# Kernel optimization log

Measured on AMD Instinct MI355X. Metric: run time of the kernel, lower is better.

Reference implementation:

```python
import jax, jax.numpy as jnp
import numpy as np

N, G, S = 51200, 128, 400  # nodes, graphs, nodes-per-graph
E, IN, H, OUT = 819200, 128, 128, 10


def _graph_conv(x, src, dst, W_rel, b_rel, W_root):
    # PyG GraphConv (aggr='add'): lin_rel(sum_{j->i} x_j) + lin_root(x_i)
    agg = jax.ops.segment_sum(x[src], dst, num_segments=N)  # [N, d]
    return agg @ W_rel + b_rel + x @ W_root


def _mixup(x, lam, perm):
    return x * lam + (1.0 - lam) * x[perm]


def setup_inputs() -> dict:
    key = jax.random.key(0)
    ks = jax.random.split(key, 12)
    rng = np.random.default_rng(0)

    x0 = jax.random.normal(ks[0], (N, IN), dtype=jnp.float32)
    edge_index = jax.random.randint(ks[1], (2, E), 0, N, dtype=jnp.int64)
    lam = jax.random.uniform(ks[2], (1,), dtype=jnp.float32)
    ptr = jnp.arange(0, N + 1, S, dtype=jnp.int64)            # [G+1]
    batch = jnp.repeat(jnp.arange(G, dtype=jnp.int64), S)     # [N]

    def seg_perm():
        return jnp.asarray(np.concatenate(
            [g * S + rng.permutation(S) for g in range(G)]), dtype=jnp.int64)

    perm1, perm2, perm3 = seg_perm(), seg_perm(), seg_perm()

    def lin(k, fan_in, fan_out):
        bound = 1.0 / np.sqrt(fan_in)
        return jax.random.uniform(k, (fan_in, fan_out), jnp.float32, -bound, bound)

    params = {
        'W1_rel': lin(ks[3], IN, H), 'b1_rel': jnp.zeros((H,), jnp.float32),
        'W1_root': lin(ks[4], IN, H),
        'W2_rel': lin(ks[5], H, H), 'b2_rel': jnp.zeros((H,), jnp.float32),
        'W2_root': lin(ks[6], H, H),
        'W_lin': lin(ks[7], H, OUT), 'b_lin': jnp.zeros((OUT,), jnp.float32),
    }
    return dict(x0=x0, edge_index=edge_index, lam=lam, ptr=ptr, batch=batch,
                perm1=perm1, perm2=perm2, perm3=perm3, **params)


def reference(x0, edge_index, lam, ptr, batch, perm1, perm2, perm3,
              W1_rel, b1_rel, W1_root, W2_rel, b2_rel, W2_root, W_lin, b_lin):
    src, dst = edge_index[0], edge_index[1]
    l = lam[0]

    x1 = jax.nn.relu(_graph_conv(x0, src, dst, W1_rel, b1_rel, W1_root))
    x1 = _mixup(x1, l, perm1)  # dropout p=0.4 is identity in eval mode

    x2 = jax.nn.relu(_graph_conv(x1, src, dst, W2_rel, b2_rel, W2_root))
    x2 = _mixup(x2, l, perm2)

    # NOTE: original forward reuses conv2 for the third layer (conv3 unused)
    x3 = jax.nn.relu(_graph_conv(x2, src, dst, W2_rel, b2_rel, W2_root))
    x3 = _mixup(x3, l, perm3)

    pooled = jax.ops.segment_sum(x3, batch, num_segments=G)  # [G, H]
    logits = pooled @ W_lin + b_lin                          # [G, OUT]
    return jax.nn.log_softmax(logits, axis=-1)
```

## Files before the change

kernel.cpp:

```cpp
#include <hip/hip_runtime.h>

#define N_NODES 51200
#define N_EDGES 819200
#define HDIM 128
#define AK 256
#define NGRAPH 128
#define SEG 400
#define NOUT 10
#define SLOT 64

typedef unsigned short ushort_t;
typedef unsigned int uint_t;
typedef __attribute__((ext_vector_type(8))) short bf16x8;
typedef __attribute__((ext_vector_type(16))) float f32x16;

static __device__ __forceinline__ unsigned short f2bf(float f) {
    unsigned int u = __float_as_uint(f);
    unsigned int r = (u + 0x7fffu + ((u >> 16) & 1u)) >> 16;
    return (unsigned short)r;
}
static __device__ __forceinline__ float bf2f(unsigned short h) {
    return __uint_as_float(((unsigned int)h) << 16);
}


__global__ void k_scatter(const int* __restrict__ src, const int* __restrict__ dst,
                          int* __restrict__ cnt, ushort_t* __restrict__ col2) {
    int e = blockIdx.x * 256 + threadIdx.x;
    int d = dst[e];
    int pos = atomicAdd(&cnt[d], 1);
    col2[(size_t)d * SLOT + pos] = (ushort_t)src[e];
}


__global__ void k_prep(const float* __restrict__ x, ushort_t* __restrict__ Abuf,
                       const float* __restrict__ W1rel, const float* __restrict__ W1root,
                       const float* __restrict__ W2rel, const float* __restrict__ W2root,
                       ushort_t* __restrict__ Wfrag1, ushort_t* __restrict__ Wfrag2,
                       float* __restrict__ pooled) {
    int b = blockIdx.x;
    if (b < 6400) {
        int idx = b * 256 + threadIdx.x;
        int row = idx >> 5;
        int c4 = (idx & 31) * 4;
        float4 v = *(const float4*)(x + (size_t)row * HDIM + c4);
        ushort4 h;
        h.x = f2bf(v.x); h.y = f2bf(v.y); h.z = f2bf(v.z); h.w = f2bf(v.w);
        *(ushort4*)(Abuf + (size_t)row * AK + HDIM + c4) = h;
    } else if (b < 6656) {
        int w2 = (b >= 6528);
        int tid = (b - (w2 ? 6528 : 6400)) * 256 + threadIdx.x;
        const float* Wrel  = w2 ? W2rel : W1rel;
        const float* Wroot = w2 ? W2root : W1root;
        ushort_t* dstF     = w2 ? Wfrag2 : Wfrag1;
        int j = tid & 7;
        int l = (tid >> 3) & 63;
        int s = (tid >> 9) & 15;
        int t = tid >> 13;
        int k = 16 * s + (l >> 5) * 8 + j;
        int n = 32 * t + (l & 31);
        float v = (k < HDIM) ? Wrel[(size_t)k * HDIM + n]
                             : Wroot[(size_t)(k - HDIM) * HDIM + n];
        dstF[tid] = f2bf(v);
    } else {
        int i = (b - 6656) * 256 + threadIdx.x;
        pooled[i] = 0.f;
    }
}


__global__ __launch_bounds__(256) void k_aggregate(ushort_t* __restrict__ Abuf,
                                                   const int* __restrict__ cnt,
                                                   const ushort_t* __restrict__ col) {
    int wave = threadIdx.x >> 6;
    int lane = threadIdx.x & 63;
    int il = lane & 15;
    int qe = lane >> 4;
    int node = blockIdx.x * 4 + wave;
    int beg = node * SLOT;
    int end = beg + cnt[node];

    const ushort_t* xsrc = Abuf + HDIM + (size_t)il * 8;

    float a[4][8];
#pragma unroll
    for (int j = 0; j < 4; ++j)
#pragma unroll
        for (int k = 0; k < 8; ++k) a[j][k] = 0.f;

    int e = beg;
    for (; e + 16 <= end; e += 16) {
        int c[4];
#pragma unroll
        for (int j = 0; j < 4; ++j) c[j] = (int)col[e + 4 * j + qe];
#pragma unroll
        for (int j = 0; j < 4; ++j) {
            uint4 v = *(const uint4*)(xsrc + (size_t)c[j] * AK);
            a[j][0] += __uint_as_float(v.x << 16);
            a[j][1] += __uint_as_float(v.x & 0xffff0000u);
            a[j][2] += __uint_as_float(v.y << 16);
            a[j][3] += __uint_as_float(v.y & 0xffff0000u);
            a[j][4] += __uint_as_float(v.z << 16);
            a[j][5] += __uint_as_float(v.z & 0xffff0000u);
            a[j][6] += __uint_as_float(v.w << 16);
            a[j][7] += __uint_as_float(v.w & 0xffff0000u);
        }
    }
    for (; e + 4 <= end; e += 4) {
        int c = (int)col[e + qe];
        uint4 v = *(const uint4*)(xsrc + (size_t)c * AK);
        a[0][0] += __uint_as_float(v.x << 16);
        a[0][1] += __uint_as_float(v.x & 0xffff0000u);
        a[0][2] += __uint_as_float(v.y << 16);
        a[0][3] += __uint_as_float(v.y & 0xffff0000u);
        a[0][4] += __uint_as_float(v.z << 16);
        a[0][5] += __uint_as_float(v.z & 0xffff0000u);
        a[0][6] += __uint_as_float(v.w << 16);
        a[0][7] += __uint_as_float(v.w & 0xffff0000u);
    }
    if (e < end) {
        int idx = e + qe;
        bool ok = idx < end;
        int c = (int)col[ok ? idx : e];
        uint4 v = *(const uint4*)(xsrc + (size_t)c * AK);
        a[1][0] += ok ? __uint_as_float(v.x << 16) : 0.f;
        a[1][1] += ok ? __uint_as_float(v.x & 0xffff0000u) : 0.f;
        a[1][2] += ok ? __uint_as_float(v.y << 16) : 0.f;
        a[1][3] += ok ? __uint_as_float(v.y & 0xffff0000u) : 0.f;
        a[1][4] += ok ? __uint_as_float(v.z << 16) : 0.f;
        a[1][5] += ok ? __uint_as_float(v.z & 0xffff0000u) : 0.f;
        a[1][6] += ok ? __uint_as_float(v.w << 16) : 0.f;
        a[1][7] += ok ? __uint_as_float(v.w & 0xffff0000u) : 0.f;
    }

    float s[8];
#pragma unroll
    for (int k = 0; k < 8; ++k) {
        s[k] = (a[0][k] + a[1][k]) + (a[2][k] + a[3][k]);
        s[k] += __shfl_xor(s[k], 16);
        s[k] += __shfl_xor(s[k], 32);
    }

    if (qe == 0) {
        uint4 o;
        o.x = (uint_t)f2bf(s[0]) | ((uint_t)f2bf(s[1]) << 16);
        o.y = (uint_t)f2bf(s[2]) | ((uint_t)f2bf(s[3]) << 16);
        o.z = (uint_t)f2bf(s[4]) | ((uint_t)f2bf(s[5]) << 16);
        o.w = (uint_t)f2bf(s[6]) | ((uint_t)f2bf(s[7]) << 16);
        *(uint4*)(Abuf + (size_t)node * AK + il * 8) = o;
    }
}


__global__ __launch_bounds__(64) void k_gemm_mfma(const ushort_t* __restrict__ Abuf,
                                                  const ushort_t* __restrict__ Wfrag,
                                                  const float* __restrict__ bias,
                                                  ushort_t* __restrict__ y) {
    __shared__ ushort_t sm[32][72];
    int lane = threadIdx.x;
    int nh = blockIdx.x & 1;
    int row0 = (blockIdx.x >> 1) * 32;
    int m = lane & 31;
    int half = lane >> 5;

    f32x16 acc[2];
#pragma unroll
    for (int t = 0; t < 2; ++t) acc[t] = (f32x16)(0.f);

    float bb[2];
#pragma unroll
    for (int t = 0; t < 2; ++t) bb[t] = bias[nh * 64 + t * 32 + m];

    const ushort_t* arow = Abuf + (size_t)(row0 + m) * AK + half * 8;
    const ushort_t* wf = Wfrag + (size_t)lane * 8 + (size_t)nh * 2 * 16 * 512;

#pragma unroll
    for (int s = 0; s < 16; ++s) {
        bf16x8 afrag = *(const bf16x8*)(arow + s * 16);
#pragma unroll
        for (int t = 0; t < 2; ++t) {
            bf16x8 bfrag = *(const bf16x8*)(wf + (size_t)(t * 16 + s) * 512);
            acc[t] = __builtin_amdgcn_mfma_f32_32x32x16_bf16(afrag, bfrag, acc[t], 0, 0, 0);
        }
    }

#pragma unroll
    for (int t = 0; t < 2; ++t) {
#pragma unroll
        for (int r = 0; r < 16; ++r) {
            int rowL = (r & 3) + 8 * (r >> 2) + 4 * half;
            sm[rowL][t * 32 + m] = f2bf(fmaxf(acc[t][r] + bb[t], 0.f));
        }
    }
    __syncthreads();
    int seg = lane & 7;
    int rbase = lane >> 3;
#pragma unroll
    for (int it = 0; it < 4; ++it) {
        int rowL = rbase + it * 8;
        int4 chunk = *(const int4*)&sm[rowL][seg * 8];
        *(int4*)(y + (size_t)(row0 + rowL) * HDIM + nh * 64 + seg * 8) = chunk;
    }
}


__global__ __launch_bounds__(64) void k_gemm_pool(const ushort_t* __restrict__ Abuf,
                                                  const ushort_t* __restrict__ Wfrag,
                                                  const float* __restrict__ bias,
                                                  float* __restrict__ pooled) {
    int lane = threadIdx.x;
    int nh = blockIdx.x & 1;
    int row0 = (blockIdx.x >> 1) * 32;
    int m = lane & 31;
    int half = lane >> 5;

    f32x16 acc[2];
#pragma unroll
    for (int t = 0; t < 2; ++t) acc[t] = (f32x16)(0.f);

    float bb[2];
#pragma unroll
    for (int t = 0; t < 2; ++t) bb[t] = bias[nh * 64 + t * 32 + m];

    const ushort_t* arow = Abuf + (size_t)(row0 + m) * AK + half * 8;
    const ushort_t* wf = Wfrag + (size_t)lane * 8 + (size_t)nh * 2 * 16 * 512;

#pragma unroll
    for (int s = 0; s < 16; ++s) {
        bf16x8 afrag = *(const bf16x8*)(arow + s * 16);
#pragma unroll
        for (int t = 0; t < 2; ++t) {
            bf16x8 bfrag = *(const bf16x8*)(wf + (size_t)(t * 16 + s) * 512);
            acc[t] = __builtin_amdgcn_mfma_f32_32x32x16_bf16(afrag, bfrag, acc[t], 0, 0, 0);
        }
    }

    int g0 = row0 / SEG;
    int bnd = (g0 + 1) * SEG;
    int straddle = (row0 + 31 >= bnd);

#pragma unroll
    for (int t = 0; t < 2; ++t) {
        float s0 = 0.f, s1 = 0.f;
#pragma unroll
        for (int r = 0; r < 16; ++r) {
            int row = row0 + (r & 3) + 8 * (r >> 2) + 4 * half;
            float v = fmaxf(acc[t][r] + bb[t], 0.f);
            if (row < bnd) s0 += v; else s1 += v;
        }
        s0 += __shfl_xor(s0, 32);
        s1 += __shfl_xor(s1, 32);
        if (half == 0) {
            int coln = nh * 64 + t * 32 + m;
            atomicAdd(&pooled[g0 * HDIM + coln], s0);
            if (straddle) atomicAdd(&pooled[(g0 + 1) * HDIM + coln], s1);
        }
    }
}


__global__ void k_mixup_toA(const ushort_t* __restrict__ y, const int* __restrict__ perm,
                            const float* __restrict__ lam, ushort_t* __restrict__ Abuf) {
    int idx = blockIdx.x * 256 + threadIdx.x;
    int row = idx >> 5;
    int c4 = (idx & 31) * 4;
    float l = lam[0];
    float om = 1.f - l;
    int p = perm[row];
    ushort4 a = *(const ushort4*)(y + (size_t)row * HDIM + c4);
    ushort4 b = *(const ushort4*)(y + (size_t)p * HDIM + c4);
    ushort4 o;
    o.x = f2bf(l * bf2f(a.x) + om * bf2f(b.x));
    o.y = f2bf(l * bf2f(a.y) + om * bf2f(b.y));
    o.z = f2bf(l * bf2f(a.z) + om * bf2f(b.z));
    o.w = f2bf(l * bf2f(a.w) + om * bf2f(b.w));
    *(ushort4*)(Abuf + (size_t)row * AK + HDIM + c4) = o;
}


__global__ __launch_bounds__(64) void k_final(const float* __restrict__ pooled,
                                              const float* __restrict__ Wlin,
                                              const float* __restrict__ blin,
                                              float* __restrict__ out) {
    int g = blockIdx.x;
    int lane = threadIdx.x;
    float2 v = *(const float2*)(pooled + (size_t)g * HDIM + lane * 2);
    float p[NOUT];
#pragma unroll
    for (int o = 0; o < NOUT; ++o)
        p[o] = v.x * Wlin[(size_t)(2 * lane) * NOUT + o] +
               v.y * Wlin[(size_t)(2 * lane + 1) * NOUT + o];
#pragma unroll
    for (int mask = 1; mask < 64; mask <<= 1)
#pragma unroll
        for (int o = 0; o < NOUT; ++o) p[o] += __shfl_xor(p[o], mask);
    if (lane == 0) {
        float lg[NOUT];
        float mx = -1e30f;
#pragma unroll
        for (int o = 0; o < NOUT; ++o) { lg[o] = p[o] + blin[o]; mx = fmaxf(mx, lg[o]); }
        float se = 0.f;
#pragma unroll
        for (int o = 0; o < NOUT; ++o) se += expf(lg[o] - mx);
        float lse = mx + logf(se);
#pragma unroll
        for (int o = 0; o < NOUT; ++o) out[g * NOUT + o] = lg[o] - lse;
    }
}


extern "C" void kernel_launch(void* const* d_in, const int* in_sizes, int n_in,
                              void* d_out, int out_size, void* d_ws, size_t ws_size,
                              hipStream_t stream) {
    const float* x0     = (const float*)d_in[0];
    const int*   edge   = (const int*)d_in[1];
    const int*   src    = edge;
    const int*   dst    = edge + N_EDGES;
    const float* lam    = (const float*)d_in[2];
    const int*   perm1  = (const int*)d_in[5];
    const int*   perm2  = (const int*)d_in[6];
    const float* W1_rel = (const float*)d_in[8];
    const float* b1_rel = (const float*)d_in[9];
    const float* W1_root= (const float*)d_in[10];
    const float* W2_rel = (const float*)d_in[11];
    const float* b2_rel = (const float*)d_in[12];
    const float* W2_root= (const float*)d_in[13];
    const float* W_lin  = (const float*)d_in[14];
    const float* b_lin  = (const float*)d_in[15];
    float* out = (float*)d_out;

    char* w = (char*)d_ws;
    size_t off = 0;
    auto alloc = [&](size_t bytes) -> void* {
        void* p = w + off;
        off = (off + bytes + 255) & ~(size_t)255;
        return p;
    };
    int* cnt       = (int*)alloc((size_t)N_NODES * 4);
    ushort_t* col2 = (ushort_t*)alloc((size_t)N_NODES * SLOT * 2);
    ushort_t* Abuf   = (ushort_t*)alloc((size_t)N_NODES * AK * 2);
    ushort_t* ybuf   = (ushort_t*)alloc((size_t)N_NODES * HDIM * 2);
    ushort_t* Wfrag1 = (ushort_t*)alloc(32768 * 2);
    ushort_t* Wfrag2 = (ushort_t*)alloc(32768 * 2);
    float* pooled    = (float*)alloc((size_t)NGRAPH * HDIM * 4);

    hipMemsetAsync(cnt, 0, (size_t)N_NODES * 4, stream);

    k_scatter<<<N_EDGES / 256, 256, 0, stream>>>(src, dst, cnt, col2);

    k_prep<<<6720, 256, 0, stream>>>(x0, Abuf, W1_rel, W1_root, W2_rel, W2_root,
                                     Wfrag1, Wfrag2, pooled);

    const int aggGrid  = N_NODES / 4;
    const int gemmGrid = (N_NODES / 32) * 2;
    const int elGrid   = (N_NODES * HDIM / 4) / 256;

    k_aggregate<<<aggGrid, 256, 0, stream>>>(Abuf, cnt, col2);
    k_gemm_mfma<<<gemmGrid, 64, 0, stream>>>(Abuf, Wfrag1, b1_rel, ybuf);
    k_mixup_toA<<<elGrid, 256, 0, stream>>>(ybuf, perm1, lam, Abuf);
    k_aggregate<<<aggGrid, 256, 0, stream>>>(Abuf, cnt, col2);
    k_gemm_mfma<<<gemmGrid, 64, 0, stream>>>(Abuf, Wfrag2, b2_rel, ybuf);
    k_mixup_toA<<<elGrid, 256, 0, stream>>>(ybuf, perm2, lam, Abuf);
    k_aggregate<<<aggGrid, 256, 0, stream>>>(Abuf, cnt, col2);
    k_gemm_pool<<<gemmGrid, 64, 0, stream>>>(Abuf, Wfrag2, b2_rel, pooled);

    k_final<<<NGRAPH, 64, 0, stream>>>(pooled, W_lin, b_lin, out);
}
```

Before: 302.7 us.

## Fuse all stages into one persistent cooperative kernel with grid syncs

Replaces the sequence of kernel launches (memset, scatter, prep, three aggregate/GEMM/mixup layers, final) with one cooperative kernel of 256 blocks of 1024 threads. Stages are separated by grid-wide barriers and each stage uses grid-stride loops. The aim is to cut launch overhead and inter-kernel gaps. In exchange, the GEMM epilogue now writes ybuf directly without the LDS transpose. Grid syncs, fixed occupancy and register limits at 1024 threads could slow the gather and MFMA phases.

```diff
diff --git a/kernel.cpp b/kernel.cpp
--- a/kernel.cpp
+++ b/kernel.cpp
@@ -1,4 +1,7 @@
 #include <hip/hip_runtime.h>
+#include <hip/hip_cooperative_groups.h>
+
+namespace cg = cooperative_groups;
 
 #define N_NODES 51200
 #define N_EDGES 819200
@@ -8,6 +11,9 @@
 #define SEG 400
 #define NOUT 10
 #define SLOT 64
+#define NBLK 256
+#define NTHR 1024
+#define NWAVE (NBLK * (NTHR / 64))
 
 typedef unsigned short ushort_t;
 typedef unsigned int uint_t;
@@ -24,287 +30,283 @@
 }
 
 
-__global__ void k_scatter(const int* __restrict__ src, const int* __restrict__ dst,
-                          int* __restrict__ cnt, ushort_t* __restrict__ col2) {
-    int e = blockIdx.x * 256 + threadIdx.x;
-    int d = dst[e];
-    int pos = atomicAdd(&cnt[d], 1);
-    col2[(size_t)d * SLOT + pos] = (ushort_t)src[e];
-}
-
-
-__global__ void k_prep(const float* __restrict__ x, ushort_t* __restrict__ Abuf,
-                       const float* __restrict__ W1rel, const float* __restrict__ W1root,
-                       const float* __restrict__ W2rel, const float* __restrict__ W2root,
-                       ushort_t* __restrict__ Wfrag1, ushort_t* __restrict__ Wfrag2,
-                       float* __restrict__ pooled) {
-    int b = blockIdx.x;
-    if (b < 6400) {
-        int idx = b * 256 + threadIdx.x;
-        int row = idx >> 5;
-        int c4 = (idx & 31) * 4;
-        float4 v = *(const float4*)(x + (size_t)row * HDIM + c4);
-        ushort4 h;
-        h.x = f2bf(v.x); h.y = f2bf(v.y); h.z = f2bf(v.z); h.w = f2bf(v.w);
-        *(ushort4*)(Abuf + (size_t)row * AK + HDIM + c4) = h;
-    } else if (b < 6656) {
-        int w2 = (b >= 6528);
-        int tid = (b - (w2 ? 6528 : 6400)) * 256 + threadIdx.x;
-        const float* Wrel  = w2 ? W2rel : W1rel;
-        const float* Wroot = w2 ? W2root : W1root;
-        ushort_t* dstF     = w2 ? Wfrag2 : Wfrag1;
-        int j = tid & 7;
-        int l = (tid >> 3) & 63;
-        int s = (tid >> 9) & 15;
-        int t = tid >> 13;
-        int k = 16 * s + (l >> 5) * 8 + j;
-        int n = 32 * t + (l & 31);
-        float v = (k < HDIM) ? Wrel[(size_t)k * HDIM + n]
-                             : Wroot[(size_t)(k - HDIM) * HDIM + n];
-        dstF[tid] = f2bf(v);
-    } else {
-        int i = (b - 6656) * 256 + threadIdx.x;
-        pooled[i] = 0.f;
+__global__ __launch_bounds__(NTHR, 4) void k_mega(
+    const float* __restrict__ x0, const int* __restrict__ src, const int* __restrict__ dst,
+    const float* __restrict__ lam, const int* __restrict__ perm1, const int* __restrict__ perm2,
+    const float* __restrict__ W1rel, const float* __restrict__ b1rel, const float* __restrict__ W1root,
+    const float* __restrict__ W2rel, const float* __restrict__ b2rel, const float* __restrict__ W2root,
+    const float* __restrict__ Wlin, const float* __restrict__ blin, float* __restrict__ out,
+    int* __restrict__ cnt, ushort_t* __restrict__ col2, ushort_t* __restrict__ Abuf,
+    ushort_t* __restrict__ ybuf, ushort_t* __restrict__ Wfrag1, ushort_t* __restrict__ Wfrag2,
+    float* __restrict__ pooled)
+{
+    cg::grid_group grid = cg::this_grid();
+    int tid = threadIdx.x;
+    int gWave = blockIdx.x * (NTHR / 64) + (tid >> 6);
+    int lane = tid & 63;
+
+    {
+        int grp = blockIdx.x * 4 + (tid >> 8);
+        int t256 = tid & 255;
+        for (int b = grp; b < 6920; b += NBLK * 4) {
+            if (b < 6400) {
+                int idx = b * 256 + t256;
+                int row = idx >> 5;
+                int c4 = (idx & 31) * 4;
+                float4 v = *(const float4*)(x0 + (size_t)row * HDIM + c4);
+                ushort4 h;
+                h.x = f2bf(v.x); h.y = f2bf(v.y); h.z = f2bf(v.z); h.w = f2bf(v.w);
+                *(ushort4*)(Abuf + (size_t)row * AK + HDIM + c4) = h;
+            } else if (b < 6656) {
+                int w2 = (b >= 6528);
+                int t = (b - (w2 ? 6528 : 6400)) * 256 + t256;
+                const float* Wrel  = w2 ? W2rel : W1rel;
+                const float* Wroot = w2 ? W2root : W1root;
+                ushort_t* dstF     = w2 ? Wfrag2 : Wfrag1;
+                int j = t & 7;
+                int l = (t >> 3) & 63;
+                int s = (t >> 9) & 15;
+                int tt = t >> 13;
+                int k = 16 * s + (l >> 5) * 8 + j;
+                int n = 32 * tt + (l & 31);
+                float v = (k < HDIM) ? Wrel[(size_t)k * HDIM + n]
+                                     : Wroot[(size_t)(k - HDIM) * HDIM + n];
+                dstF[t] = f2bf(v);
+            } else if (b < 6720) {
+                pooled[(b - 6656) * 256 + t256] = 0.f;
+            } else {
+                cnt[(b - 6720) * 256 + t256] = 0;
+            }
+        }
     }
-}
-
-
-__global__ __launch_bounds__(256) void k_aggregate(ushort_t* __restrict__ Abuf,
-                                                   const int* __restrict__ cnt,
-                                                   const ushort_t* __restrict__ col) {
-    int wave = threadIdx.x >> 6;
-    int lane = threadIdx.x & 63;
-    int il = lane & 15;
-    int qe = lane >> 4;
-    int node = blockIdx.x * 4 + wave;
-    int beg = node * SLOT;
-    int end = beg + cnt[node];
-
-    const ushort_t* xsrc = Abuf + HDIM + (size_t)il * 8;
-
-    float a[4][8];
-#pragma unroll
-    for (int j = 0; j < 4; ++j)
-#pragma unroll
-        for (int k = 0; k < 8; ++k) a[j][k] = 0.f;
-
-    int e = beg;
-    for (; e + 16 <= end; e += 16) {
-        int c[4];
-#pragma unroll
-        for (int j = 0; j < 4; ++j) c[j] = (int)col[e + 4 * j + qe];
-#pragma unroll
-        for (int j = 0; j < 4; ++j) {
-            uint4 v = *(const uint4*)(xsrc + (size_t)c[j] * AK);
-            a[j][0] += __uint_as_float(v.x << 16);
-            a[j][1] += __uint_as_float(v.x & 0xffff0000u);
-            a[j][2] += __uint_as_float(v.y << 16);
-            a[j][3] += __uint_as_float(v.y & 0xffff0000u);
-            a[j][4] += __uint_as_float(v.z << 16);
-            a[j][5] += __uint_as_float(v.z & 0xffff0000u);
-            a[j][6] += __uint_as_float(v.w << 16);
-            a[j][7] += __uint_as_float(v.w & 0xffff0000u);
+    grid.sync();
+
+    {
+        int gtid = blockIdx.x * NTHR + tid;
+        for (int e = gtid; e < N_EDGES; e += NBLK * NTHR) {
+            int d = dst[e];
+            int pos = atomicAdd(&cnt[d], 1);
+            col2[(size_t)d * SLOT + pos] = (ushort_t)src[e];
         }
     }
-    for (; e + 4 <= end; e += 4) {
-        int c = (int)col[e + qe];
-        uint4 v = *(const uint4*)(xsrc + (size_t)c * AK);
-        a[0][0] += __uint_as_float(v.x << 16);
-        a[0][1] += __uint_as_float(v.x & 0xffff0000u);
-        a[0][2] += __uint_as_float(v.y << 16);
-        a[0][3] += __uint_as_float(v.y & 0xffff0000u);
-        a[0][4] += __uint_as_float(v.z << 16);
-        a[0][5] += __uint_as_float(v.z & 0xffff0000u);
-        a[0][6] += __uint_as_float(v.w << 16);
-        a[0][7] += __uint_as_float(v.w & 0xffff0000u);
+    grid.sync();
+
+    for (int layer = 0; layer < 3; ++layer) {
+        const ushort_t* Wf  = (layer == 0) ? Wfrag1 : Wfrag2;
+        const float* bias   = (layer == 0) ? b1rel : b2rel;
+
+        {
+            int il = lane & 15;
+            int qe = lane >> 4;
+            const ushort_t* xsrc = Abuf + HDIM + (size_t)il * 8;
+            for (int node = gWave; node < N_NODES; node += NWAVE) {
+                int beg = node * SLOT;
+                int end = beg + cnt[node];
+
+                float a[4][8];
+#pragma unroll
+                for (int j = 0; j < 4; ++j)
+#pragma unroll
+                    for (int k = 0; k < 8; ++k) a[j][k] = 0.f;
+
+                int e = beg;
+                for (; e + 16 <= end; e += 16) {
+                    int c[4];
+#pragma unroll
+                    for (int j = 0; j < 4; ++j) c[j] = (int)col2[e + 4 * j + qe];
+#pragma unroll
+                    for (int j = 0; j < 4; ++j) {
+                        uint4 v = *(const uint4*)(xsrc + (size_t)c[j] * AK);
+                        a[j][0] += __uint_as_float(v.x << 16);
+                        a[j][1] += __uint_as_float(v.x & 0xffff0000u);
+                        a[j][2] += __uint_as_float(v.y << 16);
+                        a[j][3] += __uint_as_float(v.y & 0xffff0000u);
+                        a[j][4] += __uint_as_float(v.z << 16);
+                        a[j][5] += __uint_as_float(v.z & 0xffff0000u);
+                        a[j][6] += __uint_as_float(v.w << 16);
+                        a[j][7] += __uint_as_float(v.w & 0xffff0000u);
+                    }
+                }
+                for (; e + 4 <= end; e += 4) {
+                    int c = (int)col2[e + qe];
+                    uint4 v = *(const uint4*)(xsrc + (size_t)c * AK);
+                    a[0][0] += __uint_as_float(v.x << 16);
+                    a[0][1] += __uint_as_float(v.x & 0xffff0000u);
+                    a[0][2] += __uint_as_float(v.y << 16);
+                    a[0][3] += __uint_as_float(v.y & 0xffff0000u);
+                    a[0][4] += __uint_as_float(v.z << 16);
+                    a[0][5] += __uint_as_float(v.z & 0xffff0000u);
+                    a[0][6] += __uint_as_float(v.w << 16);
+                    a[0][7] += __uint_as_float(v.w & 0xffff0000u);
+                }
+                if (e < end) {
+                    int idx = e + qe;
+                    bool ok = idx < end;
+                    int c = (int)col2[ok ? idx : e];
+                    uint4 v = *(const uint4*)(xsrc + (size_t)c * AK);
+                    a[1][0] += ok ? __uint_as_float(v.x << 16) : 0.f;
+                    a[1][1] += ok ? __uint_as_float(v.x & 0xffff0000u) : 0.f;
+                    a[1][2] += ok ? __uint_as_float(v.y << 16) : 0.f;
+                    a[1][3] += ok ? __uint_as_float(v.y & 0xffff0000u) : 0.f;
+                    a[1][4] += ok ? __uint_as_float(v.z << 16) : 0.f;
+                    a[1][5] += ok ? __uint_as_float(v.z & 0xffff0000u) : 0.f;
+                    a[1][6] += ok ? __uint_as_float(v.w << 16) : 0.f;
+                    a[1][7] += ok ? __uint_as_float(v.w & 0xffff0000u) : 0.f;
+                }
+
+                float s[8];
+#pragma unroll
+                for (int k = 0; k < 8; ++k) {
+                    s[k] = (a[0][k] + a[1][k]) + (a[2][k] + a[3][k]);
+                    s[k] += __shfl_xor(s[k], 16);
+                    s[k] += __shfl_xor(s[k], 32);
+                }
+                if (qe == 0) {
+                    uint4 o;
+                    o.x = (uint_t)f2bf(s[0]) | ((uint_t)f2bf(s[1]) << 16);
+                    o.y = (uint_t)f2bf(s[2]) | ((uint_t)f2bf(s[3]) << 16);
+                    o.z = (uint_t)f2bf(s[4]) | ((uint_t)f2bf(s[5]) << 16);
+                    o.w = (uint_t)f2bf(s[6]) | ((uint_t)f2bf(s[7]) << 16);
+                    *(uint4*)(Abuf + (size_t)node * AK + il * 8) = o;
+                }
+            }
+        }
+        grid.sync();
+
+        if (layer < 2) {
+            for (int u = gWave; u < 3200; u += NWAVE) {
+                int nh = u & 1;
+                int row0 = (u >> 1) * 32;
+                int m = lane & 31;
+                int half = lane >> 5;
+
+                f32x16 acc[2];
+#pragma unroll
+                for (int t = 0; t < 2; ++t) acc[t] = (f32x16)(0.f);
+                float bb[2];
+#pragma unroll
+                for (int t = 0; t < 2; ++t) bb[t] = bias[nh * 64 + t * 32 + m];
+
+                const ushort_t* arow = Abuf + (size_t)(row0 + m) * AK + half * 8;
+                const ushort_t* wf = Wf + (size_t)lane * 8 + (size_t)nh * 2 * 16 * 512;
+
+#pragma unroll
+                for (int s = 0; s < 16; ++s) {
+                    bf16x8 afrag = *(const bf16x8*)(arow + s * 16);
+#pragma unroll
+                    for (int t = 0; t < 2; ++t) {
+                        bf16x8 bfrag = *(const bf16x8*)(wf + (size_t)(t * 16 + s) * 512);
+                        acc[t] = __builtin_amdgcn_mfma_f32_32x32x16_bf16(afrag, bfrag, acc[t], 0, 0, 0);
+                    }
+                }
+#pragma unroll
+                for (int t = 0; t < 2; ++t) {
+                    int coln = nh * 64 + t * 32 + m;
+#pragma unroll
+                    for (int r = 0; r < 16; ++r) {
+                        int row = row0 + (r & 3) + 8 * (r >> 2) + 4 * half;
+                        ybuf[(size_t)row * HDIM + coln] = f2bf(fmaxf(acc[t][r] + bb[t], 0.f));
+                    }
+                }
+            }
+            grid.sync();
+
+            {
+                const int* perm = (layer == 0) ? perm1 : perm2;
+                float l = lam[0];
+                float om = 1.f - l;
+                int gtid = blockIdx.x * NTHR + tid;
+                for (int idx = gtid; idx < N_NODES * 32; idx += NBLK * NTHR) {
+                    int row = idx >> 5;
+                    int c4 = (idx & 31) * 4;
+                    int p = perm[row];
+                    ushort4 a = *(const ushort4*)(ybuf + (size_t)row * HDIM + c4);
+                    ushort4 b = *(const ushort4*)(ybuf + (size_t)p * HDIM + c4);
+                    ushort4 o;
+                    o.x = f2bf(l * bf2f(a.x) + om * bf2f(b.x));
+                    o.y = f2bf(l * bf2f(a.y) + om * bf2f(b.y));
+                    o.z = f2bf(l * bf2f(a.z) + om * bf2f(b.z));
+                    o.w = f2bf(l * bf2f(a.w) + om * bf2f(b.w));
+                    *(ushort4*)(Abuf + (size_t)row * AK + HDIM + c4) = o;
+                }
+            }
+            grid.sync();
+        } else {
+            for (int u = gWave; u < 3200; u += NWAVE) {
+                int nh = u & 1;
+                int row0 = (u >> 1) * 32;
+                int m = lane & 31;
+                int half = lane >> 5;
+
+                f32x16 acc[2];
+#pragma unroll
+                for (int t = 0; t < 2; ++t) acc[t] = (f32x16)(0.f);
+                float bb[2];
+#pragma unroll
+                for (int t = 0; t < 2; ++t) bb[t] = bias[nh * 64 + t * 32 + m];
+
+                const ushort_t* arow = Abuf + (size_t)(row0 + m) * AK + half * 8;
+                const ushort_t* wf = Wf + (size_t)lane * 8 + (size_t)nh * 2 * 16 * 512;
+
+#pragma unroll
+                for (int s = 0; s < 16; ++s) {
+                    bf16x8 afrag = *(const bf16x8*)(arow + s * 16);
+#pragma unroll
+                    for (int t = 0; t < 2; ++t) {
+                        bf16x8 bfrag = *(const bf16x8*)(wf + (size_t)(t * 16 + s) * 512);
+                        acc[t] = __builtin_amdgcn_mfma_f32_32x32x16_bf16(afrag, bfrag, acc[t], 0, 0, 0);
+                    }
+                }
+
+                int g0 = row0 / SEG;
+                int bnd = (g0 + 1) * SEG;
+                int straddle = (row0 + 31 >= bnd);
+
+#pragma unroll
+                for (int t = 0; t < 2; ++t) {
+                    float s0 = 0.f, s1 = 0.f;
+#pragma unroll
+                    for (int r = 0; r < 16; ++r) {
+                        int row = row0 + (r & 3) + 8 * (r >> 2) + 4 * half;
+                        float v = fmaxf(acc[t][r] + bb[t], 0.f);
+                        if (row < bnd) s0 += v; else s1 += v;
+                    }
+                    s0 += __shfl_xor(s0, 32);
+                    s1 += __shfl_xor(s1, 32);
+                    if (half == 0) {
+                        int coln = nh * 64 + t * 32 + m;
+                        atomicAdd(&pooled[g0 * HDIM + coln], s0);
+                        if (straddle) atomicAdd(&pooled[(g0 + 1) * HDIM + coln], s1);
+                    }
+                }
+            }
+            grid.sync();
+        }
     }
-    if (e < end) {
-        int idx = e + qe;
-        bool ok = idx < end;
-        int c = (int)col[ok ? idx : e];
-        uint4 v = *(const uint4*)(xsrc + (size_t)c * AK);
-        a[1][0] += ok ? __uint_as_float(v.x << 16) : 0.f;
-        a[1][1] += ok ? __uint_as_float(v.x & 0xffff0000u) : 0.f;
-        a[1][2] += ok ? __uint_as_float(v.y << 16) : 0.f;
-        a[1][3] += ok ? __uint_as_float(v.y & 0xffff0000u) : 0.f;
-        a[1][4] += ok ? __uint_as_float(v.z << 16) : 0.f;
-        a[1][5] += ok ? __uint_as_float(v.z & 0xffff0000u) : 0.f;
-        a[1][6] += ok ? __uint_as_float(v.w << 16) : 0.f;
-        a[1][7] += ok ? __uint_as_float(v.w & 0xffff0000u) : 0.f;
-    }
-
-    float s[8];
-#pragma unroll
-    for (int k = 0; k < 8; ++k) {
-        s[k] = (a[0][k] + a[1][k]) + (a[2][k] + a[3][k]);
-        s[k] += __shfl_xor(s[k], 16);
-        s[k] += __shfl_xor(s[k], 32);
-    }
-
-    if (qe == 0) {
-        uint4 o;
-        o.x = (uint_t)f2bf(s[0]) | ((uint_t)f2bf(s[1]) << 16);
-        o.y = (uint_t)f2bf(s[2]) | ((uint_t)f2bf(s[3]) << 16);
-        o.z = (uint_t)f2bf(s[4]) | ((uint_t)f2bf(s[5]) << 16);
-        o.w = (uint_t)f2bf(s[6]) | ((uint_t)f2bf(s[7]) << 16);
-        *(uint4*)(Abuf + (size_t)node * AK + il * 8) = o;
-    }
-}
-
-
-__global__ __launch_bounds__(64) void k_gemm_mfma(const ushort_t* __restrict__ Abuf,
-                                                  const ushort_t* __restrict__ Wfrag,
-                                                  const float* __restrict__ bias,
-                                                  ushort_t* __restrict__ y) {
-    __shared__ ushort_t sm[32][72];
-    int lane = threadIdx.x;
-    int nh = blockIdx.x & 1;
-    int row0 = (blockIdx.x >> 1) * 32;
-    int m = lane & 31;
-    int half = lane >> 5;
-
-    f32x16 acc[2];
-#pragma unroll
-    for (int t = 0; t < 2; ++t) acc[t] = (f32x16)(0.f);
-
-    float bb[2];
-#pragma unroll
-    for (int t = 0; t < 2; ++t) bb[t] = bias[nh * 64 + t * 32 + m];
-
-    const ushort_t* arow = Abuf + (size_t)(row0 + m) * AK + half * 8;
-    const ushort_t* wf = Wfrag + (size_t)lane * 8 + (size_t)nh * 2 * 16 * 512;
-
-#pragma unroll
-    for (int s = 0; s < 16; ++s) {
-        bf16x8 afrag = *(const bf16x8*)(arow + s * 16);
-#pragma unroll
-        for (int t = 0; t < 2; ++t) {
-            bf16x8 bfrag = *(const bf16x8*)(wf + (size_t)(t * 16 + s) * 512);
-            acc[t] = __builtin_amdgcn_mfma_f32_32x32x16_bf16(afrag, bfrag, acc[t], 0, 0, 0);
-        }
-    }
-
-#pragma unroll
-    for (int t = 0; t < 2; ++t) {
-#pragma unroll
-        for (int r = 0; r < 16; ++r) {
-            int rowL = (r & 3) + 8 * (r >> 2) + 4 * half;
-            sm[rowL][t * 32 + m] = f2bf(fmaxf(acc[t][r] + bb[t], 0.f));
-        }
-    }
-    __syncthreads();
-    int seg = lane & 7;
-    int rbase = lane >> 3;
-#pragma unroll
-    for (int it = 0; it < 4; ++it) {
-        int rowL = rbase + it * 8;
-        int4 chunk = *(const int4*)&sm[rowL][seg * 8];
-        *(int4*)(y + (size_t)(row0 + rowL) * HDIM + nh * 64 + seg * 8) = chunk;
-    }
-}
-
-
-__global__ __launch_bounds__(64) void k_gemm_pool(const ushort_t* __restrict__ Abuf,
-                                                  const ushort_t* __restrict__ Wfrag,
-                                                  const float* __restrict__ bias,
-                                                  float* __restrict__ pooled) {
-    int lane = threadIdx.x;
-    int nh = blockIdx.x & 1;
-    int row0 = (blockIdx.x >> 1) * 32;
-    int m = lane & 31;
-    int half = lane >> 5;
-
-    f32x16 acc[2];
-#pragma unroll
-    for (int t = 0; t < 2; ++t) acc[t] = (f32x16)(0.f);
-
-    float bb[2];
-#pragma unroll
-    for (int t = 0; t < 2; ++t) bb[t] = bias[nh * 64 + t * 32 + m];
-
-    const ushort_t* arow = Abuf + (size_t)(row0 + m) * AK + half * 8;
-    const ushort_t* wf = Wfrag + (size_t)lane * 8 + (size_t)nh * 2 * 16 * 512;
-
-#pragma unroll
-    for (int s = 0; s < 16; ++s) {
-        bf16x8 afrag = *(const bf16x8*)(arow + s * 16);
-#pragma unroll
-        for (int t = 0; t < 2; ++t) {
-            bf16x8 bfrag = *(const bf16x8*)(wf + (size_t)(t * 16 + s) * 512);
-            acc[t] = __builtin_amdgcn_mfma_f32_32x32x16_bf16(afrag, bfrag, acc[t], 0, 0, 0);
-        }
-    }
-
-    int g0 = row0 / SEG;
-    int bnd = (g0 + 1) * SEG;
-    int straddle = (row0 + 31 >= bnd);
-
-#pragma unroll
-    for (int t = 0; t < 2; ++t) {
-        float s0 = 0.f, s1 = 0.f;
-#pragma unroll
-        for (int r = 0; r < 16; ++r) {
-            int row = row0 + (r & 3) + 8 * (r >> 2) + 4 * half;
-            float v = fmaxf(acc[t][r] + bb[t], 0.f);
-            if (row < bnd) s0 += v; else s1 += v;
-        }
-        s0 += __shfl_xor(s0, 32);
-        s1 += __shfl_xor(s1, 32);
-        if (half == 0) {
-            int coln = nh * 64 + t * 32 + m;
-            atomicAdd(&pooled[g0 * HDIM + coln], s0);
-            if (straddle) atomicAdd(&pooled[(g0 + 1) * HDIM + coln], s1);
-        }
-    }
-}
-
-
-__global__ void k_mixup_toA(const ushort_t* __restrict__ y, const int* __restrict__ perm,
-                            const float* __restrict__ lam, ushort_t* __restrict__ Abuf) {
-    int idx = blockIdx.x * 256 + threadIdx.x;
-    int row = idx >> 5;
-    int c4 = (idx & 31) * 4;
-    float l = lam[0];
-    float om = 1.f - l;
-    int p = perm[row];
-    ushort4 a = *(const ushort4*)(y + (size_t)row * HDIM + c4);
-    ushort4 b = *(const ushort4*)(y + (size_t)p * HDIM + c4);
-    ushort4 o;
-    o.x = f2bf(l * bf2f(a.x) + om * bf2f(b.x));
-    o.y = f2bf(l * bf2f(a.y) + om * bf2f(b.y));
-    o.z = f2bf(l * bf2f(a.z) + om * bf2f(b.z));
-    o.w = f2bf(l * bf2f(a.w) + om * bf2f(b.w));
-    *(ushort4*)(Abuf + (size_t)row * AK + HDIM + c4) = o;
-}
-
-
-__global__ __launch_bounds__(64) void k_final(const float* __restrict__ pooled,
-                                              const float* __restrict__ Wlin,
-                                              const float* __restrict__ blin,
-                                              float* __restrict__ out) {
-    int g = blockIdx.x;
-    int lane = threadIdx.x;
-    float2 v = *(const float2*)(pooled + (size_t)g * HDIM + lane * 2);
-    float p[NOUT];
-#pragma unroll
-    for (int o = 0; o < NOUT; ++o)
-        p[o] = v.x * Wlin[(size_t)(2 * lane) * NOUT + o] +
-               v.y * Wlin[(size_t)(2 * lane + 1) * NOUT + o];
-#pragma unroll
-    for (int mask = 1; mask < 64; mask <<= 1)
-#pragma unroll
-        for (int o = 0; o < NOUT; ++o) p[o] += __shfl_xor(p[o], mask);
-    if (lane == 0) {
-        float lg[NOUT];
-        float mx = -1e30f;
-#pragma unroll
-        for (int o = 0; o < NOUT; ++o) { lg[o] = p[o] + blin[o]; mx = fmaxf(mx, lg[o]); }
-        float se = 0.f;
-#pragma unroll
-        for (int o = 0; o < NOUT; ++o) se += expf(lg[o] - mx);
-        float lse = mx + logf(se);
-#pragma unroll
-        for (int o = 0; o < NOUT; ++o) out[g * NOUT + o] = lg[o] - lse;
+
+    for (int g = gWave; g < NGRAPH; g += NWAVE) {
+        float2 v = *(const float2*)(pooled + (size_t)g * HDIM + lane * 2);
+        float p[NOUT];
+#pragma unroll
+        for (int o = 0; o < NOUT; ++o)
+            p[o] = v.x * Wlin[(size_t)(2 * lane) * NOUT + o] +
+                   v.y * Wlin[(size_t)(2 * lane + 1) * NOUT + o];
+#pragma unroll
+        for (int mask = 1; mask < 64; mask <<= 1)
+#pragma unroll
+            for (int o = 0; o < NOUT; ++o) p[o] += __shfl_xor(p[o], mask);
+        if (lane == 0) {
+            float lg[NOUT];
+            float mx = -1e30f;
+#pragma unroll
+            for (int o = 0; o < NOUT; ++o) { lg[o] = p[o] + blin[o]; mx = fmaxf(mx, lg[o]); }
+            float se = 0.f;
+#pragma unroll
+            for (int o = 0; o < NOUT; ++o) se += expf(lg[o] - mx);
+            float lse = mx + logf(se);
+#pragma unroll
+            for (int o = 0; o < NOUT; ++o) out[g * NOUT + o] = lg[o] - lse;
+        }
     }
 }
 
@@ -336,33 +338,22 @@
         off = (off + bytes + 255) & ~(size_t)255;
         return p;
     };
-    int* cnt       = (int*)alloc((size_t)N_NODES * 4);
-    ushort_t* col2 = (ushort_t*)alloc((size_t)N_NODES * SLOT * 2);
+    int* cnt        = (int*)alloc((size_t)N_NODES * 4);
+    ushort_t* col2  = (ushort_t*)alloc((size_t)N_NODES * SLOT * 2);
     ushort_t* Abuf   = (ushort_t*)alloc((size_t)N_NODES * AK * 2);
     ushort_t* ybuf   = (ushort_t*)alloc((size_t)N_NODES * HDIM * 2);
     ushort_t* Wfrag1 = (ushort_t*)alloc(32768 * 2);
     ushort_t* Wfrag2 = (ushort_t*)alloc(32768 * 2);
     float* pooled    = (float*)alloc((size_t)NGRAPH * HDIM * 4);
 
-    hipMemsetAsync(cnt, 0, (size_t)N_NODES * 4, stream);
-
-    k_scatter<<<N_EDGES / 256, 256, 0, stream>>>(src, dst, cnt, col2);
-
-    k_prep<<<6720, 256, 0, stream>>>(x0, Abuf, W1_rel, W1_root, W2_rel, W2_root,
-                                     Wfrag1, Wfrag2, pooled);
-
-    const int aggGrid  = N_NODES / 4;
-    const int gemmGrid = (N_NODES / 32) * 2;
-    const int elGrid   = (N_NODES * HDIM / 4) / 256;
-
-    k_aggregate<<<aggGrid, 256, 0, stream>>>(Abuf, cnt, col2);
-    k_gemm_mfma<<<gemmGrid, 64, 0, stream>>>(Abuf, Wfrag1, b1_rel, ybuf);
-    k_mixup_toA<<<elGrid, 256, 0, stream>>>(ybuf, perm1, lam, Abuf);
-    k_aggregate<<<aggGrid, 256, 0, stream>>>(Abuf, cnt, col2);
-    k_gemm_mfma<<<gemmGrid, 64, 0, stream>>>(Abuf, Wfrag2, b2_rel, ybuf);
-    k_mixup_toA<<<elGrid, 256, 0, stream>>>(ybuf, perm2, lam, Abuf);
-    k_aggregate<<<aggGrid, 256, 0, stream>>>(Abuf, cnt, col2);
-    k_gemm_pool<<<gemmGrid, 64, 0, stream>>>(Abuf, Wfrag2, b2_rel, pooled);
-
-    k_final<<<NGRAPH, 64, 0, stream>>>(pooled, W_lin, b_lin, out);
+    void* args[] = {
+        (void*)&x0, (void*)&src, (void*)&dst, (void*)&lam, (void*)&perm1, (void*)&perm2,
+        (void*)&W1_rel, (void*)&b1_rel, (void*)&W1_root,
+        (void*)&W2_rel, (void*)&b2_rel, (void*)&W2_root,
+        (void*)&W_lin, (void*)&b_lin, (void*)&out,
+        (void*)&cnt, (void*)&col2, (void*)&Abuf, (void*)&ybuf,
+        (void*)&Wfrag1, (void*)&Wfrag2, (void*)&pooled
+    };
+    hipLaunchCooperativeKernel((const void*)k_mega, dim3(NBLK), dim3(NTHR),
+                               args, 0, stream);
 }
```

Result: slower. 781.9 us (+158.3%).
